# Performance work log

Hardware: AMD Instinct MI355X
Metric: run time of the kernel (lower is better)

The kernel has to match this reference:

```python
import jax, jax.numpy as jnp
import numpy as np

SR = 44100
PRE_EMPH = 0.97
FRAME_LEN = int(0.02 * SR)      # 882
FRAME_HOP = FRAME_LEN // 2      # 441
N_FFT = 2048
EPS = 1e-10


def setup_inputs() -> dict:
    key = jax.random.key(0)
    k1, k2 = jax.random.split(key)
    waveform = jax.random.normal(k1, (16, 441000), dtype=jnp.float32)
    # librosa mel filterbank is a fixed nonnegative (n_mels, n_fft//2+1) matrix;
    # a random surrogate keeps the math (dense matmul) identical.
    mel_filters = jax.random.uniform(k2, (60, N_FFT // 2 + 1), dtype=jnp.float32)
    return {"waveform": waveform, "mel_filters": mel_filters}


def _mfdwc(waveform, mel_filters):
    dt = waveform.dtype
    # pre-emphasis: y[0]=x[0], y[t]=x[t]-0.97*x[t-1]
    emph = jnp.concatenate(
        [waveform[:, :1], waveform[:, 1:] - PRE_EMPH * waveform[:, :-1]], axis=1)
    L = emph.shape[1]
    n_frames = 1 + (L - FRAME_LEN) // FRAME_HOP  # static
    idx = jnp.arange(n_frames)[:, None] * FRAME_HOP + jnp.arange(FRAME_LEN)[None, :]
    frames = emph[:, idx]                                   # (B, T, 882)
    window = jnp.asarray(np.hamming(FRAME_LEN), dtype=dt)   # (882,)
    windowed = frames * window
    spec = jnp.fft.rfft(windowed, n=N_FFT, axis=-1)         # (B, T, 1025) complex
    power = jnp.real(spec) ** 2 + jnp.imag(spec) ** 2       # |FFT|^2
    mel = jnp.einsum('mf,btf->btm', mel_filters, power)     # (B, T, 60)
    logmel = jnp.log(mel + EPS)
    # 1-level Haar DWT along mel axis (pywt convention, even length):
    # cA = (x_even + x_odd)/sqrt(2), cD = (x_even - x_odd)/sqrt(2)
    sq2 = jnp.sqrt(jnp.asarray(2.0, dt))
    x_even, x_odd = logmel[..., 0::2], logmel[..., 1::2]
    cA = (x_even + x_odd) / sq2                             # (B, T, 30)
    cD = (x_even - x_odd) / sq2                             # (B, T, 30)
    # delta (window=3, edge-padded): d[t] = a[clamp(t+1)] - a[clamp(t-1)]
    fwd = jnp.concatenate([cA[:, 1:], cA[:, -1:]], axis=1)
    bwd = jnp.concatenate([cA[:, :1], cA[:, :-1]], axis=1)
    delta = fwd - bwd
    feats = jnp.concatenate([cA, delta, cD], axis=-1)       # (B, T, 90)
    mean = jnp.mean(feats, axis=1)
    std = jnp.std(feats, axis=1, ddof=1)                    # torch.std unbiased
    return jnp.concatenate([mean, std], axis=1)             # (B, 180)


def reference(waveform, mel_filters):
    return _mfdwc(waveform, mel_filters)
```

## Files before the change

kernel.cpp:

```cpp
#include <hip/hip_runtime.h>
#include <hip/hip_bf16.h>
#include <math.h>

#define FRAME_LEN 882
#define FRAME_HOP 441
#define NFFT 2048
#define NFRAMES 999
#define NBATCH 16
#define NMEL 60
#define WAVE_LEN 441000
#define PRE_EMPH 0.97f
#define EPS 1e-10f
#define NROWS (NBATCH * NFRAMES)
#define KPAD 1056
#define PI_F 3.14159265358979323846f

#define PADI(i) ((i) + ((i) >> 4))

__device__ __forceinline__ float2 cadd(float2 a, float2 b){ return make_float2(a.x+b.x, a.y+b.y); }
__device__ __forceinline__ float2 csub(float2 a, float2 b){ return make_float2(a.x-b.x, a.y-b.y); }
__device__ __forceinline__ float2 cmul(float2 a, float2 b){ return make_float2(a.x*b.x - a.y*b.y, a.x*b.y + a.y*b.x); }
__device__ __forceinline__ float2 tw(float ang){ float s, c; __sincosf(ang, &s, &c); return make_float2(c, s); }

#define DIF_GROUP(S)                                                        \
  {                                                                         \
    const float fr = (float)r;                                              \
    _Pragma("unroll")                                                       \
    for (int k = 0; k < 4; ++k) {                                           \
      float2 wk = tw(-PI_F * ((float)(k*(S)) + fr) / (float)(4*(S)));       \
      float2 u = x[k], v = x[k+4];                                          \
      x[k] = cadd(u, v); x[k+4] = cmul(csub(u, v), wk);                     \
    }                                                                       \
    {                                                                       \
      float2 w0 = tw(-PI_F * fr / (float)(2*(S)));                          \
      float2 w1 = tw(-PI_F * ((float)(S) + fr) / (float)(2*(S)));           \
      float2 u, v;                                                          \
      u=x[0]; v=x[2]; x[0]=cadd(u,v); x[2]=cmul(csub(u,v), w0);             \
      u=x[1]; v=x[3]; x[1]=cadd(u,v); x[3]=cmul(csub(u,v), w1);             \
      u=x[4]; v=x[6]; x[4]=cadd(u,v); x[6]=cmul(csub(u,v), w0);             \
      u=x[5]; v=x[7]; x[5]=cadd(u,v); x[7]=cmul(csub(u,v), w1);             \
    }                                                                       \
    {                                                                       \
      float2 w0 = tw(-PI_F * fr / (float)(S));                              \
      float2 u, v;                                                          \
      u=x[0]; v=x[1]; x[0]=cadd(u,v); x[1]=cmul(csub(u,v), w0);             \
      u=x[2]; v=x[3]; x[2]=cadd(u,v); x[3]=cmul(csub(u,v), w0);             \
      u=x[4]; v=x[5]; x[4]=cadd(u,v); x[5]=cmul(csub(u,v), w0);             \
      u=x[6]; v=x[7]; x[6]=cadd(u,v); x[7]=cmul(csub(u,v), w0);             \
    }                                                                       \
  }

__device__ __forceinline__ void dif_radix4(float2* x) {
  float2 y0 = cadd(x[0], x[2]);
  float2 y2 = csub(x[0], x[2]);
  float2 y1 = cadd(x[1], x[3]);
  float2 t3 = csub(x[1], x[3]);
  float2 y3 = make_float2(t3.y, -t3.x);
  x[0] = cadd(y0, y1); x[1] = csub(y0, y1);
  x[2] = cadd(y2, y3); x[3] = csub(y2, y3);
}

__global__ __launch_bounds__(256) void fft_pow_kernel(
    const float* __restrict__ wav, __hip_bfloat16* __restrict__ powr)
{
  __shared__ float2 lds[NFFT + (NFFT >> 4)];
  const int t  = threadIdx.x;
  const int t0 = 2 * blockIdx.x, t1 = t0 + 1;
  const bool has1 = (t1 < NFRAMES);
  const int b = blockIdx.y;
  const float* w = wav + (size_t)b * WAVE_LEN;
  const int s0 = t0 * FRAME_HOP, s1 = t1 * FRAME_HOP;

  float2 x[8];
#pragma unroll
  for (int k = 0; k < 8; ++k) {
    int i = k * 256 + t;
    float v1 = 0.f, v2 = 0.f;
    if (i < FRAME_LEN) {
      float win = 0.54f - 0.46f * __cosf(6.283185307179586f * (float)i / 881.0f);
      int s = s0 + i;
      float e1 = (s > 0) ? (w[s] - PRE_EMPH * w[s - 1]) : w[s];
      v1 = e1 * win;
      if (has1) {
        int ss = s1 + i;
        v2 = (w[ss] - PRE_EMPH * w[ss - 1]) * win;
      }
    }
    x[k] = make_float2(v1, v2);
  }

  { const int r = t; DIF_GROUP(256) }
#pragma unroll
  for (int k = 0; k < 8; ++k) lds[PADI(k * 256 + t)] = x[k];
  __syncthreads();

  {
    const int q = t >> 5, r = t & 31;
#pragma unroll
    for (int k = 0; k < 8; ++k) x[k] = lds[PADI(q * 256 + k * 32 + r)];
    DIF_GROUP(32)
#pragma unroll
    for (int k = 0; k < 8; ++k) lds[PADI(q * 256 + k * 32 + r)] = x[k];
  }
  __syncthreads();

  {
    const int q = t >> 2, r = t & 3;
#pragma unroll
    for (int k = 0; k < 8; ++k) x[k] = lds[PADI(q * 32 + k * 4 + r)];
    DIF_GROUP(4)
#pragma unroll
    for (int k = 0; k < 8; ++k) lds[PADI(q * 32 + k * 4 + r)] = x[k];
  }
  __syncthreads();

  {
    float2 xa[4], xb[4];
#pragma unroll
    for (int j = 0; j < 4; ++j) {
      xa[j] = lds[PADI(4 * t + j)];
      xb[j] = lds[PADI(4 * (t + 256) + j)];
    }
    dif_radix4(xa);
    dif_radix4(xb);
#pragma unroll
    for (int j = 0; j < 4; ++j) {
      lds[PADI(4 * t + j)] = xa[j];
      lds[PADI(4 * (t + 256) + j)] = xb[j];
    }
  }
  __syncthreads();

  const size_t row0 = (size_t)b * NFRAMES + t0;
  __hip_bfloat16* p0 = powr + row0 * KPAD;
  __hip_bfloat16* p1 = powr + (row0 + 1) * KPAD;
#pragma unroll
  for (int c = 0; c < 5; ++c) {
    int f = t + 256 * c;
    bool valid = (c < 4) || (t == 0);
    if (c == 4) f = 1024;
    if (valid) {
      int j1 = (int)(__brev((unsigned)f) >> 21);
      int j2 = (int)(__brev((unsigned)((NFFT - f) & (NFFT - 1))) >> 21);
      float2 z = lds[PADI(j1)];
      float2 y = lds[PADI(j2)];
      float f1r = z.x + y.x, f1i = z.y - y.y;
      float f2r = z.y + y.y, f2i = y.x - z.x;
      float pw1 = 0.25f * (f1r * f1r + f1i * f1i);
      float pw2 = 0.25f * (f2r * f2r + f2i * f2i);
      p0[f] = __float2bfloat16(pw1);
      if (has1) p1[f] = __float2bfloat16(pw2);
    }
  }
  if (t < KPAD - 1025) {
    p0[1025 + t] = __float2bfloat16(0.f);
    if (has1) p1[1025 + t] = __float2bfloat16(0.f);
  }
}

__global__ __launch_bounds__(256) void filtconv_kernel(
    const float* __restrict__ filt, __hip_bfloat16* __restrict__ filtb)
{
  const int m = blockIdx.x;
  for (int k = threadIdx.x; k < KPAD; k += 256) {
    float v = (m < NMEL && k < 1025) ? filt[m * 1025 + k] : 0.f;
    filtb[(size_t)m * KPAD + k] = __float2bfloat16(v);
  }
}

typedef __attribute__((ext_vector_type(8))) short short8x;
typedef __attribute__((ext_vector_type(4))) float float4x;

__global__ __launch_bounds__(256) void melgemm_kernel(
    const __hip_bfloat16* __restrict__ powr,
    const __hip_bfloat16* __restrict__ filtb,
    float* __restrict__ logmel)
{
  const int wave = threadIdx.x >> 6, lane = threadIdx.x & 63;
  const int row0 = blockIdx.x * 32;
  const int melbase = wave * 16;
  const int lrow = lane & 15, kgrp = lane >> 4;

  int r0 = row0 + lrow;        if (r0 > NROWS - 1) r0 = NROWS - 1;
  int r1 = row0 + 16 + lrow;   if (r1 > NROWS - 1) r1 = NROWS - 1;
  const __hip_bfloat16* a0p = powr + (size_t)r0 * KPAD + kgrp * 8;
  const __hip_bfloat16* a1p = powr + (size_t)r1 * KPAD + kgrp * 8;
  const __hip_bfloat16* bp  = filtb + (size_t)(melbase + lrow) * KPAD + kgrp * 8;

  float4x acc0 = {0.f, 0.f, 0.f, 0.f};
  float4x acc1 = {0.f, 0.f, 0.f, 0.f};
  for (int kk = 0; kk < KPAD; kk += 32) {
    short8x a0 = *(const short8x*)a0p;
    short8x a1 = *(const short8x*)a1p;
    short8x bf = *(const short8x*)bp;
    acc0 = __builtin_amdgcn_mfma_f32_16x16x32_bf16(a0, bf, acc0, 0, 0, 0);
    acc1 = __builtin_amdgcn_mfma_f32_16x16x32_bf16(a1, bf, acc1, 0, 0, 0);
    a0p += 32; a1p += 32; bp += 32;
  }

  const int mel = melbase + (lane & 15);
  const int rsub = (lane >> 4) * 4;
  if (mel < NMEL) {
#pragma unroll
    for (int reg = 0; reg < 4; ++reg) {
      int rowA = row0 + rsub + reg;
      if (rowA < NROWS) logmel[(size_t)rowA * NMEL + mel] = __logf(acc0[reg] + EPS);
      int rowB = rowA + 16;
      if (rowB < NROWS) logmel[(size_t)rowB * NMEL + mel] = __logf(acc1[reg] + EPS);
    }
  }
}

__global__ __launch_bounds__(256) void stats_kernel(
    const float* __restrict__ logmel, float* __restrict__ out)
{
  __shared__ float red[4];
  const int j   = blockIdx.x;
  const int b   = blockIdx.y;
  const int tid = threadIdx.x;
  const float* lm = logmel + (size_t)b * NFRAMES * NMEL;
  const float inv_sq2 = 0.7071067811865475f;

  float fv[4];
  int   nf = 0;
#pragma unroll
  for (int r = 0; r < 4; ++r) {
    int tt = tid + (r << 8);
    if (tt < NFRAMES) {
      float v;
      if (j < 30) {
        int m = j;
        v = (lm[tt * NMEL + 2 * m] + lm[tt * NMEL + 2 * m + 1]) * inv_sq2;
      } else if (j < 60) {
        int m  = j - 30;
        int tp = (tt + 1 > NFRAMES - 1) ? (NFRAMES - 1) : (tt + 1);
        int tm = (tt - 1 < 0) ? 0 : (tt - 1);
        float ca_p = (lm[tp * NMEL + 2 * m] + lm[tp * NMEL + 2 * m + 1]) * inv_sq2;
        float ca_m = (lm[tm * NMEL + 2 * m] + lm[tm * NMEL + 2 * m + 1]) * inv_sq2;
        v = ca_p - ca_m;
      } else {
        int m = j - 60;
        v = (lm[tt * NMEL + 2 * m] - lm[tt * NMEL + 2 * m + 1]) * inv_sq2;
      }
      fv[nf++] = v;
    }
  }

  float s = 0.f;
  for (int r = 0; r < nf; ++r) s += fv[r];
  for (int o = 32; o > 0; o >>= 1) s += __shfl_xor(s, o, 64);
  if ((tid & 63) == 0) red[tid >> 6] = s;
  __syncthreads();
  float mean = (red[0] + red[1] + red[2] + red[3]) / (float)NFRAMES;
  __syncthreads();

  float s2 = 0.f;
  for (int r = 0; r < nf; ++r) { float d = fv[r] - mean; s2 += d * d; }
  for (int o = 32; o > 0; o >>= 1) s2 += __shfl_xor(s2, o, 64);
  if ((tid & 63) == 0) red[tid >> 6] = s2;
  __syncthreads();
  float var = (red[0] + red[1] + red[2] + red[3]) / (float)(NFRAMES - 1);

  if (tid == 0) {
    out[b * 180 + j]      = mean;
    out[b * 180 + 90 + j] = sqrtf(var);
  }
}

extern "C" void kernel_launch(void* const* d_in, const int* in_sizes, int n_in,
                              void* d_out, int out_size, void* d_ws, size_t ws_size,
                              hipStream_t stream) {
  const float* wav  = (const float*)d_in[0];
  const float* filt = (const float*)d_in[1];
  float* out = (float*)d_out;

  unsigned char* ws = (unsigned char*)d_ws;
  __hip_bfloat16* powr  = (__hip_bfloat16*)(ws);
  size_t off = (size_t)NROWS * KPAD * 2;
  __hip_bfloat16* filtb = (__hip_bfloat16*)(ws + off);
  off += (size_t)64 * KPAD * 2;
  float* logmel = (float*)(ws + off);

  filtconv_kernel<<<64, 256, 0, stream>>>(filt, filtb);
  fft_pow_kernel<<<dim3((NFRAMES + 1) / 2, NBATCH), 256, 0, stream>>>(wav, powr);
  melgemm_kernel<<<(NROWS + 31) / 32, 256, 0, stream>>>(powr, filtb, logmel);
  stats_kernel<<<dim3(90, NBATCH), 256, 0, stream>>>(logmel, out);
}
```

Measured before the change: 135.0 us.

## Restructure FFT as radix-16/16/8 with 128 threads and recurrence twiddles

```diff
diff --git a/kernel.cpp b/kernel.cpp
--- a/kernel.cpp
+++ b/kernel.cpp
@@ -20,113 +20,141 @@
 __device__ __forceinline__ float2 cadd(float2 a, float2 b){ return make_float2(a.x+b.x, a.y+b.y); }
 __device__ __forceinline__ float2 csub(float2 a, float2 b){ return make_float2(a.x-b.x, a.y-b.y); }
 __device__ __forceinline__ float2 cmul(float2 a, float2 b){ return make_float2(a.x*b.x - a.y*b.y, a.x*b.y + a.y*b.x); }
-__device__ __forceinline__ float2 tw(float ang){ float s, c; __sincosf(ang, &s, &c); return make_float2(c, s); }
-
-#define DIF_GROUP(S)                                                        \
-  {                                                                         \
-    const float fr = (float)r;                                              \
-    _Pragma("unroll")                                                       \
-    for (int k = 0; k < 4; ++k) {                                           \
-      float2 wk = tw(-PI_F * ((float)(k*(S)) + fr) / (float)(4*(S)));       \
-      float2 u = x[k], v = x[k+4];                                          \
-      x[k] = cadd(u, v); x[k+4] = cmul(csub(u, v), wk);                     \
-    }                                                                       \
-    {                                                                       \
-      float2 w0 = tw(-PI_F * fr / (float)(2*(S)));                          \
-      float2 w1 = tw(-PI_F * ((float)(S) + fr) / (float)(2*(S)));           \
-      float2 u, v;                                                          \
-      u=x[0]; v=x[2]; x[0]=cadd(u,v); x[2]=cmul(csub(u,v), w0);             \
-      u=x[1]; v=x[3]; x[1]=cadd(u,v); x[3]=cmul(csub(u,v), w1);             \
-      u=x[4]; v=x[6]; x[4]=cadd(u,v); x[6]=cmul(csub(u,v), w0);             \
-      u=x[5]; v=x[7]; x[5]=cadd(u,v); x[7]=cmul(csub(u,v), w1);             \
-    }                                                                       \
-    {                                                                       \
-      float2 w0 = tw(-PI_F * fr / (float)(S));                              \
-      float2 u, v;                                                          \
-      u=x[0]; v=x[1]; x[0]=cadd(u,v); x[1]=cmul(csub(u,v), w0);             \
-      u=x[2]; v=x[3]; x[2]=cadd(u,v); x[3]=cmul(csub(u,v), w0);             \
-      u=x[4]; v=x[5]; x[4]=cadd(u,v); x[5]=cmul(csub(u,v), w0);             \
-      u=x[6]; v=x[7]; x[6]=cadd(u,v); x[7]=cmul(csub(u,v), w0);             \
-    }                                                                       \
-  }
-
-__device__ __forceinline__ void dif_radix4(float2* x) {
-  float2 y0 = cadd(x[0], x[2]);
-  float2 y2 = csub(x[0], x[2]);
-  float2 y1 = cadd(x[1], x[3]);
-  float2 t3 = csub(x[1], x[3]);
-  float2 y3 = make_float2(t3.y, -t3.x);
-  x[0] = cadd(y0, y1); x[1] = csub(y0, y1);
-  x[2] = cadd(y2, y3); x[3] = csub(y2, y3);
-}
-
-__global__ __launch_bounds__(256) void fft_pow_kernel(
+__device__ __forceinline__ float2 rotni(float2 z){ return make_float2(z.y, -z.x); }
+
+__device__ __forceinline__ void dif_group16(float2* x, float2 t1) {
+  const float2 C81 = make_float2(0.9238795325f, -0.3826834324f);
+  const float2 C82 = make_float2(0.7071067812f, -0.7071067812f);
+  const float2 C83 = make_float2(0.3826834324f, -0.9238795325f);
+  float2 w0 = t1, w1 = cmul(t1, C81), w2 = cmul(t1, C82), w3 = cmul(t1, C83);
+  float2 ws1[8] = {w0, w1, w2, w3, rotni(w0), rotni(w1), rotni(w2), rotni(w3)};
+#pragma unroll
+  for (int k = 0; k < 8; ++k) {
+    float2 u = x[k], v = x[k + 8];
+    x[k] = cadd(u, v);
+    x[k + 8] = cmul(csub(u, v), ws1[k]);
+  }
+  float2 t2 = cmul(t1, t1);
+  float2 v1 = cmul(t2, C82);
+  float2 ws2[4] = {t2, v1, rotni(t2), rotni(v1)};
+#pragma unroll
+  for (int h = 0; h < 2; ++h) {
+#pragma unroll
+    for (int k = 0; k < 4; ++k) {
+      float2 u = x[h*8 + k], v = x[h*8 + k + 4];
+      x[h*8 + k] = cadd(u, v);
+      x[h*8 + k + 4] = cmul(csub(u, v), ws2[k]);
+    }
+  }
+  float2 t4 = cmul(t2, t2);
+  float2 t4r = rotni(t4);
+#pragma unroll
+  for (int h = 0; h < 4; ++h) {
+    float2 a = x[h*4 + 0], b = x[h*4 + 2];
+    x[h*4 + 0] = cadd(a, b); x[h*4 + 2] = cmul(csub(a, b), t4);
+    a = x[h*4 + 1]; b = x[h*4 + 3];
+    x[h*4 + 1] = cadd(a, b); x[h*4 + 3] = cmul(csub(a, b), t4r);
+  }
+  float2 t8 = cmul(t4, t4);
+#pragma unroll
+  for (int j = 0; j < 8; ++j) {
+    float2 a = x[2*j], b = x[2*j + 1];
+    x[2*j] = cadd(a, b); x[2*j + 1] = cmul(csub(a, b), t8);
+  }
+}
+
+__device__ __forceinline__ void dif8(float2* y) {
+  const float2 c1 = make_float2(0.7071067812f, -0.7071067812f);
+  const float2 c3 = make_float2(-0.7071067812f, -0.7071067812f);
+  float2 u, v;
+  u=y[0]; v=y[4]; y[0]=cadd(u,v); y[4]=csub(u,v);
+  u=y[1]; v=y[5]; y[1]=cadd(u,v); y[5]=cmul(csub(u,v), c1);
+  u=y[2]; v=y[6]; y[2]=cadd(u,v); y[6]=rotni(csub(u,v));
+  u=y[3]; v=y[7]; y[3]=cadd(u,v); y[7]=cmul(csub(u,v), c3);
+  u=y[0]; v=y[2]; y[0]=cadd(u,v); y[2]=csub(u,v);
+  u=y[1]; v=y[3]; y[1]=cadd(u,v); y[3]=rotni(csub(u,v));
+  u=y[4]; v=y[6]; y[4]=cadd(u,v); y[6]=csub(u,v);
+  u=y[5]; v=y[7]; y[5]=cadd(u,v); y[7]=rotni(csub(u,v));
+  u=y[0]; v=y[1]; y[0]=cadd(u,v); y[1]=csub(u,v);
+  u=y[2]; v=y[3]; y[2]=cadd(u,v); y[3]=csub(u,v);
+  u=y[4]; v=y[5]; y[4]=cadd(u,v); y[5]=csub(u,v);
+  u=y[6]; v=y[7]; y[6]=cadd(u,v); y[7]=csub(u,v);
+}
+
+__global__ __launch_bounds__(128) void fft_pow_kernel(
     const float* __restrict__ wav, __hip_bfloat16* __restrict__ powr)
 {
   __shared__ float2 lds[NFFT + (NFFT >> 4)];
   const int t  = threadIdx.x;
-  const int t0 = 2 * blockIdx.x, t1 = t0 + 1;
-  const bool has1 = (t1 < NFRAMES);
+  const int t0 = 2 * blockIdx.x, t1f = t0 + 1;
+  const bool has1 = (t1f < NFRAMES);
   const int b = blockIdx.y;
   const float* w = wav + (size_t)b * WAVE_LEN;
-  const int s0 = t0 * FRAME_HOP, s1 = t1 * FRAME_HOP;
-
-  float2 x[8];
-#pragma unroll
-  for (int k = 0; k < 8; ++k) {
-    int i = k * 256 + t;
-    float v1 = 0.f, v2 = 0.f;
-    if (i < FRAME_LEN) {
-      float win = 0.54f - 0.46f * __cosf(6.283185307179586f * (float)i / 881.0f);
-      int s = s0 + i;
-      float e1 = (s > 0) ? (w[s] - PRE_EMPH * w[s - 1]) : w[s];
-      v1 = e1 * win;
-      if (has1) {
-        int ss = s1 + i;
-        v2 = (w[ss] - PRE_EMPH * w[ss - 1]) * win;
+  const int s0 = t0 * FRAME_HOP, s1 = t1f * FRAME_HOP;
+
+  float2 x[16];
+  {
+    float sB, cB, sD, cD;
+    __sincosf(6.283185307179586f * (float)t / 881.0f, &sB, &cB);
+    __sincosf(6.283185307179586f * 128.0f / 881.0f, &sD, &cD);
+    float2 cur  = make_float2(cB, sB);
+    float2 step = make_float2(cD, sD);
+#pragma unroll
+    for (int k = 0; k < 16; ++k) {
+      int i = k * 128 + t;
+      float v1 = 0.f, v2 = 0.f;
+      if (i < FRAME_LEN) {
+        float win = 0.54f - 0.46f * cur.x;
+        int s = s0 + i;
+        float e1 = (s > 0) ? (w[s] - PRE_EMPH * w[s - 1]) : w[s];
+        v1 = e1 * win;
+        if (has1) {
+          int ss = s1 + i;
+          v2 = (w[ss] - PRE_EMPH * w[ss - 1]) * win;
+        }
       }
-    }
-    x[k] = make_float2(v1, v2);
-  }
-
-  { const int r = t; DIF_GROUP(256) }
-#pragma unroll
-  for (int k = 0; k < 8; ++k) lds[PADI(k * 256 + t)] = x[k];
-  __syncthreads();
+      x[k] = make_float2(v1, v2);
+      cur = cmul(cur, step);
+    }
+  }
 
   {
-    const int q = t >> 5, r = t & 31;
-#pragma unroll
-    for (int k = 0; k < 8; ++k) x[k] = lds[PADI(q * 256 + k * 32 + r)];
-    DIF_GROUP(32)
-#pragma unroll
-    for (int k = 0; k < 8; ++k) lds[PADI(q * 256 + k * 32 + r)] = x[k];
-  }
+    float sA, cA;
+    __sincosf(-PI_F * (float)t / 1024.0f, &sA, &cA);
+    dif_group16(x, make_float2(cA, sA));
+  }
+#pragma unroll
+  for (int k = 0; k < 16; ++k) lds[PADI(k * 128 + t)] = x[k];
   __syncthreads();
 
   {
-    const int q = t >> 2, r = t & 3;
-#pragma unroll
-    for (int k = 0; k < 8; ++k) x[k] = lds[PADI(q * 32 + k * 4 + r)];
-    DIF_GROUP(4)
-#pragma unroll
-    for (int k = 0; k < 8; ++k) lds[PADI(q * 32 + k * 4 + r)] = x[k];
+    const int Q = t >> 3, r = t & 7;
+    const int base = Q * 128 + r;
+#pragma unroll
+    for (int k = 0; k < 16; ++k) x[k] = lds[PADI(base + k * 8)];
+    float sA, cA;
+    __sincosf(-PI_F * (float)r / 64.0f, &sA, &cA);
+    dif_group16(x, make_float2(cA, sA));
+    __syncthreads();
+#pragma unroll
+    for (int k = 0; k < 16; ++k) lds[PADI(base + k * 8)] = x[k];
   }
   __syncthreads();
 
   {
-    float2 xa[4], xb[4];
-#pragma unroll
-    for (int j = 0; j < 4; ++j) {
-      xa[j] = lds[PADI(4 * t + j)];
-      xb[j] = lds[PADI(4 * (t + 256) + j)];
-    }
-    dif_radix4(xa);
-    dif_radix4(xb);
-#pragma unroll
-    for (int j = 0; j < 4; ++j) {
-      lds[PADI(4 * t + j)] = xa[j];
-      lds[PADI(4 * (t + 256) + j)] = xb[j];
+    float2 ya[8], yb[8];
+#pragma unroll
+    for (int j = 0; j < 8; ++j) {
+      ya[j] = lds[PADI(16 * t + j)];
+      yb[j] = lds[PADI(16 * t + 8 + j)];
+    }
+    dif8(ya);
+    dif8(yb);
+    __syncthreads();
+#pragma unroll
+    for (int j = 0; j < 8; ++j) {
+      lds[PADI(16 * t + j)] = ya[j];
+      lds[PADI(16 * t + 8 + j)] = yb[j];
     }
   }
   __syncthreads();
@@ -135,10 +163,10 @@
   __hip_bfloat16* p0 = powr + row0 * KPAD;
   __hip_bfloat16* p1 = powr + (row0 + 1) * KPAD;
 #pragma unroll
-  for (int c = 0; c < 5; ++c) {
-    int f = t + 256 * c;
-    bool valid = (c < 4) || (t == 0);
-    if (c == 4) f = 1024;
+  for (int c = 0; c < 9; ++c) {
+    int f = c * 128 + t;
+    bool valid = (c < 8) || (t == 0);
+    if (c == 8) f = 1024;
     if (valid) {
       int j1 = (int)(__brev((unsigned)f) >> 21);
       int j2 = (int)(__brev((unsigned)((NFFT - f) & (NFFT - 1))) >> 21);
@@ -282,7 +310,7 @@
   float* logmel = (float*)(ws + off);
 
   filtconv_kernel<<<64, 256, 0, stream>>>(filt, filtb);
-  fft_pow_kernel<<<dim3((NFRAMES + 1) / 2, NBATCH), 256, 0, stream>>>(wav, powr);
+  fft_pow_kernel<<<dim3((NFRAMES + 1) / 2, NBATCH), 128, 0, stream>>>(wav, powr);
   melgemm_kernel<<<(NROWS + 31) / 32, 256, 0, stream>>>(powr, filtb, logmel);
   stats_kernel<<<dim3(90, NBATCH), 256, 0, stream>>>(logmel, out);
 }
```

New measurement: 134.6 us. No clear change (-0.3%).

## Derive FFT twiddles recursively and shrink mel GEMM tiles to 16 rows

Applied to the files above, without the earlier changes.

```diff
diff --git a/kernel.cpp b/kernel.cpp
--- a/kernel.cpp
+++ b/kernel.cpp
@@ -20,42 +20,34 @@
 __device__ __forceinline__ float2 cadd(float2 a, float2 b){ return make_float2(a.x+b.x, a.y+b.y); }
 __device__ __forceinline__ float2 csub(float2 a, float2 b){ return make_float2(a.x-b.x, a.y-b.y); }
 __device__ __forceinline__ float2 cmul(float2 a, float2 b){ return make_float2(a.x*b.x - a.y*b.y, a.x*b.y + a.y*b.x); }
-__device__ __forceinline__ float2 tw(float ang){ float s, c; __sincosf(ang, &s, &c); return make_float2(c, s); }
-
-#define DIF_GROUP(S)                                                        \
-  {                                                                         \
-    const float fr = (float)r;                                              \
-    _Pragma("unroll")                                                       \
-    for (int k = 0; k < 4; ++k) {                                           \
-      float2 wk = tw(-PI_F * ((float)(k*(S)) + fr) / (float)(4*(S)));       \
-      float2 u = x[k], v = x[k+4];                                          \
-      x[k] = cadd(u, v); x[k+4] = cmul(csub(u, v), wk);                     \
-    }                                                                       \
-    {                                                                       \
-      float2 w0 = tw(-PI_F * fr / (float)(2*(S)));                          \
-      float2 w1 = tw(-PI_F * ((float)(S) + fr) / (float)(2*(S)));           \
-      float2 u, v;                                                          \
-      u=x[0]; v=x[2]; x[0]=cadd(u,v); x[2]=cmul(csub(u,v), w0);             \
-      u=x[1]; v=x[3]; x[1]=cadd(u,v); x[3]=cmul(csub(u,v), w1);             \
-      u=x[4]; v=x[6]; x[4]=cadd(u,v); x[6]=cmul(csub(u,v), w0);             \
-      u=x[5]; v=x[7]; x[5]=cadd(u,v); x[7]=cmul(csub(u,v), w1);             \
-    }                                                                       \
-    {                                                                       \
-      float2 w0 = tw(-PI_F * fr / (float)(S));                              \
-      float2 u, v;                                                          \
-      u=x[0]; v=x[1]; x[0]=cadd(u,v); x[1]=cmul(csub(u,v), w0);             \
-      u=x[2]; v=x[3]; x[2]=cadd(u,v); x[3]=cmul(csub(u,v), w0);             \
-      u=x[4]; v=x[5]; x[4]=cadd(u,v); x[5]=cmul(csub(u,v), w0);             \
-      u=x[6]; v=x[7]; x[6]=cadd(u,v); x[7]=cmul(csub(u,v), w0);             \
-    }                                                                       \
-  }
+__device__ __forceinline__ float2 rotni(float2 z){ return make_float2(z.y, -z.x); }
+
+__device__ __forceinline__ void dif_group8(float2* x, float2 t1) {
+  const float2 C41 = make_float2(0.7071067812f, -0.7071067812f);
+  float2 w0 = t1, w1 = cmul(t1, C41), w2 = rotni(w0), w3 = rotni(w1);
+  float2 u, v;
+  u=x[0]; v=x[4]; x[0]=cadd(u,v); x[4]=cmul(csub(u,v), w0);
+  u=x[1]; v=x[5]; x[1]=cadd(u,v); x[5]=cmul(csub(u,v), w1);
+  u=x[2]; v=x[6]; x[2]=cadd(u,v); x[6]=cmul(csub(u,v), w2);
+  u=x[3]; v=x[7]; x[3]=cadd(u,v); x[7]=cmul(csub(u,v), w3);
+  float2 t2 = cmul(t1, t1), t2r = rotni(t2);
+  u=x[0]; v=x[2]; x[0]=cadd(u,v); x[2]=cmul(csub(u,v), t2);
+  u=x[1]; v=x[3]; x[1]=cadd(u,v); x[3]=cmul(csub(u,v), t2r);
+  u=x[4]; v=x[6]; x[4]=cadd(u,v); x[6]=cmul(csub(u,v), t2);
+  u=x[5]; v=x[7]; x[5]=cadd(u,v); x[7]=cmul(csub(u,v), t2r);
+  float2 t4 = cmul(t2, t2);
+  u=x[0]; v=x[1]; x[0]=cadd(u,v); x[1]=cmul(csub(u,v), t4);
+  u=x[2]; v=x[3]; x[2]=cadd(u,v); x[3]=cmul(csub(u,v), t4);
+  u=x[4]; v=x[5]; x[4]=cadd(u,v); x[5]=cmul(csub(u,v), t4);
+  u=x[6]; v=x[7]; x[6]=cadd(u,v); x[7]=cmul(csub(u,v), t4);
+}
 
 __device__ __forceinline__ void dif_radix4(float2* x) {
   float2 y0 = cadd(x[0], x[2]);
   float2 y2 = csub(x[0], x[2]);
   float2 y1 = cadd(x[1], x[3]);
   float2 t3 = csub(x[1], x[3]);
-  float2 y3 = make_float2(t3.y, -t3.x);
+  float2 y3 = rotni(t3);
   x[0] = cadd(y0, y1); x[1] = csub(y0, y1);
   x[2] = cadd(y2, y3); x[3] = csub(y2, y3);
 }
@@ -65,31 +57,43 @@
 {
   __shared__ float2 lds[NFFT + (NFFT >> 4)];
   const int t  = threadIdx.x;
-  const int t0 = 2 * blockIdx.x, t1 = t0 + 1;
-  const bool has1 = (t1 < NFRAMES);
+  const int t0 = 2 * blockIdx.x, t1f = t0 + 1;
+  const bool has1 = (t1f < NFRAMES);
   const int b = blockIdx.y;
   const float* w = wav + (size_t)b * WAVE_LEN;
-  const int s0 = t0 * FRAME_HOP, s1 = t1 * FRAME_HOP;
+  const int s0 = t0 * FRAME_HOP, s1 = t1f * FRAME_HOP;
 
   float2 x[8];
-#pragma unroll
-  for (int k = 0; k < 8; ++k) {
-    int i = k * 256 + t;
-    float v1 = 0.f, v2 = 0.f;
-    if (i < FRAME_LEN) {
-      float win = 0.54f - 0.46f * __cosf(6.283185307179586f * (float)i / 881.0f);
-      int s = s0 + i;
-      float e1 = (s > 0) ? (w[s] - PRE_EMPH * w[s - 1]) : w[s];
-      v1 = e1 * win;
-      if (has1) {
-        int ss = s1 + i;
-        v2 = (w[ss] - PRE_EMPH * w[ss - 1]) * win;
+  {
+    float sB, cB, sD, cD;
+    __sincosf(6.283185307179586f * (float)t / 881.0f, &sB, &cB);
+    __sincosf(6.283185307179586f * 256.0f / 881.0f, &sD, &cD);
+    float2 cur  = make_float2(cB, sB);
+    float2 step = make_float2(cD, sD);
+#pragma unroll
+    for (int k = 0; k < 8; ++k) {
+      int i = k * 256 + t;
+      float v1 = 0.f, v2 = 0.f;
+      if (i < FRAME_LEN) {
+        float win = 0.54f - 0.46f * cur.x;
+        int s = s0 + i;
+        float e1 = (s > 0) ? (w[s] - PRE_EMPH * w[s - 1]) : w[s];
+        v1 = e1 * win;
+        if (has1) {
+          int ss = s1 + i;
+          v2 = (w[ss] - PRE_EMPH * w[ss - 1]) * win;
+        }
       }
-    }
-    x[k] = make_float2(v1, v2);
-  }
-
-  { const int r = t; DIF_GROUP(256) }
+      x[k] = make_float2(v1, v2);
+      cur = cmul(cur, step);
+    }
+  }
+
+  {
+    float sA, cA;
+    __sincosf(-PI_F * (float)t / 1024.0f, &sA, &cA);
+    dif_group8(x, make_float2(cA, sA));
+  }
 #pragma unroll
   for (int k = 0; k < 8; ++k) lds[PADI(k * 256 + t)] = x[k];
   __syncthreads();
@@ -98,7 +102,10 @@
     const int q = t >> 5, r = t & 31;
 #pragma unroll
     for (int k = 0; k < 8; ++k) x[k] = lds[PADI(q * 256 + k * 32 + r)];
-    DIF_GROUP(32)
+    float sA, cA;
+    __sincosf(-PI_F * (float)r / 128.0f, &sA, &cA);
+    dif_group8(x, make_float2(cA, sA));
+    __syncthreads();
 #pragma unroll
     for (int k = 0; k < 8; ++k) lds[PADI(q * 256 + k * 32 + r)] = x[k];
   }
@@ -108,7 +115,10 @@
     const int q = t >> 2, r = t & 3;
 #pragma unroll
     for (int k = 0; k < 8; ++k) x[k] = lds[PADI(q * 32 + k * 4 + r)];
-    DIF_GROUP(4)
+    float tc = (r == 0) ? 1.0f : (r == 1) ? 0.980785280f : (r == 2) ? 0.923879533f : 0.831469612f;
+    float ts = (r == 0) ? 0.0f : (r == 1) ? -0.195090322f : (r == 2) ? -0.382683432f : -0.555570233f;
+    dif_group8(x, make_float2(tc, ts));
+    __syncthreads();
 #pragma unroll
     for (int k = 0; k < 8; ++k) lds[PADI(q * 32 + k * 4 + r)] = x[k];
   }
@@ -123,6 +133,7 @@
     }
     dif_radix4(xa);
     dif_radix4(xb);
+    __syncthreads();
 #pragma unroll
     for (int j = 0; j < 4; ++j) {
       lds[PADI(4 * t + j)] = xa[j];
@@ -177,36 +188,28 @@
     float* __restrict__ logmel)
 {
   const int wave = threadIdx.x >> 6, lane = threadIdx.x & 63;
-  const int row0 = blockIdx.x * 32;
-  const int melbase = wave * 16;
+  const int row0 = blockIdx.x * 16;
   const int lrow = lane & 15, kgrp = lane >> 4;
 
-  int r0 = row0 + lrow;        if (r0 > NROWS - 1) r0 = NROWS - 1;
-  int r1 = row0 + 16 + lrow;   if (r1 > NROWS - 1) r1 = NROWS - 1;
-  const __hip_bfloat16* a0p = powr + (size_t)r0 * KPAD + kgrp * 8;
-  const __hip_bfloat16* a1p = powr + (size_t)r1 * KPAD + kgrp * 8;
-  const __hip_bfloat16* bp  = filtb + (size_t)(melbase + lrow) * KPAD + kgrp * 8;
-
-  float4x acc0 = {0.f, 0.f, 0.f, 0.f};
-  float4x acc1 = {0.f, 0.f, 0.f, 0.f};
-  for (int kk = 0; kk < KPAD; kk += 32) {
-    short8x a0 = *(const short8x*)a0p;
-    short8x a1 = *(const short8x*)a1p;
+  const __hip_bfloat16* ap = powr + (size_t)(row0 + lrow) * KPAD + kgrp * 8;
+  const __hip_bfloat16* bp = filtb + (size_t)(wave * 16 + lrow) * KPAD + kgrp * 8;
+
+  float4x acc = {0.f, 0.f, 0.f, 0.f};
+#pragma unroll 3
+  for (int kk = 0; kk < 33; ++kk) {
+    short8x a = *(const short8x*)ap;
     short8x bf = *(const short8x*)bp;
-    acc0 = __builtin_amdgcn_mfma_f32_16x16x32_bf16(a0, bf, acc0, 0, 0, 0);
-    acc1 = __builtin_amdgcn_mfma_f32_16x16x32_bf16(a1, bf, acc1, 0, 0, 0);
-    a0p += 32; a1p += 32; bp += 32;
-  }
-
-  const int mel = melbase + (lane & 15);
+    acc = __builtin_amdgcn_mfma_f32_16x16x32_bf16(a, bf, acc, 0, 0, 0);
+    ap += 32; bp += 32;
+  }
+
+  const int mel = wave * 16 + (lane & 15);
   const int rsub = (lane >> 4) * 4;
   if (mel < NMEL) {
 #pragma unroll
     for (int reg = 0; reg < 4; ++reg) {
-      int rowA = row0 + rsub + reg;
-      if (rowA < NROWS) logmel[(size_t)rowA * NMEL + mel] = __logf(acc0[reg] + EPS);
-      int rowB = rowA + 16;
-      if (rowB < NROWS) logmel[(size_t)rowB * NMEL + mel] = __logf(acc1[reg] + EPS);
+      int row = row0 + rsub + reg;
+      logmel[(size_t)row * NMEL + mel] = __logf(acc[reg] + EPS);
     }
   }
 }
@@ -283,6 +286,6 @@
 
   filtconv_kernel<<<64, 256, 0, stream>>>(filt, filtb);
   fft_pow_kernel<<<dim3((NFRAMES + 1) / 2, NBATCH), 256, 0, stream>>>(wav, powr);
-  melgemm_kernel<<<(NROWS + 31) / 32, 256, 0, stream>>>(powr, filtb, logmel);
+  melgemm_kernel<<<NROWS / 16, 256, 0, stream>>>(powr, filtb, logmel);
   stats_kernel<<<dim3(90, NBATCH), 256, 0, stream>>>(logmel, out);
 }
```

Result: no change. 135.9 us (+0.7%).
